# Kernel optimization log

Measured on AMD Instinct MI355X. Metric: run time of the kernel, lower is better.

## Reference

```python
import jax, jax.numpy as jnp
import numpy as np

N_NODES = 100000
N_EDGES = 1600000
D_IN, D_HID, D_OUT = 128, 128, 64


def spmm(row, col, val, h, n):
    # y[i] = sum_{e: row[e]==i} val[e] * h[col[e]]  (A_hat @ h with A in COO form)
    return jax.ops.segment_sum(val[:, None] * h[col], row, num_segments=n)


def setup_inputs() -> dict:
    key = jax.random.key(0)
    ks = jax.random.split(key, 7)
    x = jax.random.normal(ks[0], (1, N_NODES, D_IN), dtype=jnp.float32)
    edge_row = jax.random.randint(ks[1], (N_EDGES,), 0, N_NODES, dtype=jnp.int32)
    edge_col = jax.random.randint(ks[2], (N_EDGES,), 0, N_NODES, dtype=jnp.int32)
    edge_val = jax.random.uniform(ks[3], (N_EDGES,), dtype=jnp.float32)
    W0 = jax.random.normal(ks[4], (D_HID, D_IN), dtype=jnp.float32) * 0.05
    W1 = jax.random.normal(ks[5], (D_HID, D_HID), dtype=jnp.float32) * 0.05
    W2 = jax.random.normal(ks[6], (D_OUT, D_HID), dtype=jnp.float32) * 0.05
    return {"x": x, "edge_row": edge_row, "edge_col": edge_col,
            "edge_val": edge_val, "W0": W0, "W1": W1, "W2": W2}


def reference(x, edge_row, edge_col, edge_val, W0, W1, W2):
    B, N, D = x.shape
    n = B * N
    h = x.reshape(n, D)
    # input conv: Linear (no bias) -> SpMM -> ReLU
    h = jax.nn.relu(spmm(edge_row, edge_col, edge_val, h @ W0.T, n))
    # hidden conv with residual: ReLU(A (h W1^T)) + h
    h = jax.nn.relu(spmm(edge_row, edge_col, edge_val, h @ W1.T, n)) + h
    # dropout is identity in eval mode
    out = spmm(edge_row, edge_col, edge_val, h @ W2.T, n)
    return out
```

## Files before the change

### kernel.cpp

```cpp
#include <hip/hip_runtime.h>


typedef unsigned int u32;
typedef unsigned short u16;
typedef __attribute__((ext_vector_type(8))) short bf16x8;
typedef __attribute__((ext_vector_type(4))) float f32x4;

constexpr int NN = 100000;
constexpr int NE = 1600000;
constexpr int PAD = 100352;
constexpr int NBUCK = 392;
constexpr int BCAP = 4608;
constexpr int EPB = 4096;
constexpr int P1B = (NE + EPB - 1) / EPB;
constexpr int G0B = (NN + 63) / 64;
constexpr int NCB = 13;

__device__ __forceinline__ u16 f2bf(float f) {
    u32 x = __float_as_uint(f);
    x += 0x7fffu + ((x >> 16) & 1u);
    return (u16)(x >> 16);
}

__device__ __forceinline__ void wfrag_one(const float* __restrict__ W,
                                          u16* __restrict__ Wf, int total, int i)
{
    if (i < total) {
        const int j    = i & 7;
        const int lane = (i >> 3) & 63;
        const int kc   = (i >> 9) & 3;
        const int ct   = i >> 11;
        const int src  = (ct * 16 + (lane & 15)) * 128 + kc * 32 + (lane >> 4) * 8 + j;
        Wf[i] = f2bf(W[src]);
    }
}

__global__ __launch_bounds__(256)
void wcvt_kernel(const float* __restrict__ W0, const float* __restrict__ W1,
                 const float* __restrict__ W2, u16* __restrict__ wf0,
                 u16* __restrict__ wf1, u16* __restrict__ wf2)
{
    const int i = blockIdx.x * 256 + threadIdx.x;
    wfrag_one(W0, wf0, 128 * 128, i);
    wfrag_one(W1, wf1, 128 * 128, i);
    wfrag_one(W2, wf2, 64 * 128, i);
}

__global__ __launch_bounds__(256)
void part1_kernel(const int* __restrict__ erow, const int* __restrict__ ecol,
                  const float* __restrict__ eval,
                  int2* __restrict__ part, int* __restrict__ boffs)
{
    __shared__ int shist[512];
    __shared__ int sexcl[512];
    __shared__ int sdat[256];
    const int tid = threadIdx.x;
    const int blk = blockIdx.x;

    shist[tid] = 0; shist[tid + 256] = 0;
    __syncthreads();

    const int base = blk * EPB;
    int rr[EPB / 256];
    #pragma unroll
    for (int j = 0; j < EPB / 256; ++j) {
        const int e = base + j * 256 + tid;
        rr[j] = (e < NE) ? erow[e] : -1;
        if (rr[j] >= 0) atomicAdd(&shist[rr[j] >> 8], 1);
    }
    __syncthreads();

    const int c0 = shist[2 * tid];
    const int c1 = shist[2 * tid + 1];
    const int tsum = c0 + c1;
    sdat[tid] = tsum;
    __syncthreads();
    #pragma unroll
    for (int off = 1; off < 256; off <<= 1) {
        const int v = (tid >= off) ? sdat[tid - off] : 0;
        __syncthreads();
        sdat[tid] += v;
        __syncthreads();
    }
    const int excl = sdat[tid] - tsum;
    sexcl[2 * tid]     = excl;
    sexcl[2 * tid + 1] = excl + c0;
    __syncthreads();

    for (int b = tid; b < NBUCK; b += 256)
        boffs[(size_t)b * P1B + blk] = sexcl[b];
    if (tid == 0) boffs[(size_t)NBUCK * P1B + blk] = sdat[255];
    __syncthreads();

    #pragma unroll
    for (int j = 0; j < EPB / 256; ++j) {
        const int r = rr[j];
        if (r >= 0) {
            const int e = base + j * 256 + tid;
            const int pos = atomicAdd(&sexcl[r >> 8], 1);
            part[(size_t)blk * EPB + pos] =
                make_int2(((r & 255) << 17) | ecol[e], __float_as_int(eval[e]));
        }
    }
}

__global__ __launch_bounds__(256)
void gemm0_kernel(const float* __restrict__ x, const u16* __restrict__ Wf,
                  u16* __restrict__ Cb)
{
    constexpr int RS   = 136;
    constexpr int PADW = 136;
    __shared__ u16 smem[64 * 136];
    u16* sA = smem;
    u16* sC = smem;
    const int tid  = threadIdx.x;
    const int w    = tid >> 6;
    const int lane = tid & 63;
    const int m    = lane & 15;
    const int q    = lane >> 4;
    const int rowBase = (int)blockIdx.x * 64;

    #pragma unroll
    for (int i = 0; i < 8; ++i) {
        const int g = (i * 256 + tid) * 4;
        const int r = g >> 7, c = g & 127;
        float4 v = make_float4(0.f, 0.f, 0.f, 0.f);
        if (rowBase + r < NN) v = *(const float4*)(x + (size_t)(rowBase + r) * 128 + c);
        u16* d = &sA[r * RS + c];
        d[0] = f2bf(v.x); d[1] = f2bf(v.y); d[2] = f2bf(v.z); d[3] = f2bf(v.w);
    }
    __syncthreads();

    bf16x8 afrag[4];
    #pragma unroll
    for (int kc = 0; kc < 4; ++kc)
        afrag[kc] = *(const bf16x8*)&sA[(w * 16 + m) * RS + kc * 32 + q * 8];
    __syncthreads();

    #pragma unroll
    for (int ct = 0; ct < 8; ++ct) {
        f32x4 acc = {0.f, 0.f, 0.f, 0.f};
        #pragma unroll
        for (int kc = 0; kc < 4; ++kc) {
            const bf16x8 b = *(const bf16x8*)(Wf + (((ct * 4 + kc) * 64) + lane) * 8);
            acc = __builtin_amdgcn_mfma_f32_16x16x32_bf16(afrag[kc], b, acc, 0, 0, 0);
        }
        #pragma unroll
        for (int r = 0; r < 4; ++r)
            sC[(w * 16 + q * 4 + r) * PADW + ct * 16 + m] = f2bf(acc[r]);
    }
    __syncthreads();

    const int g    = lane >> 2;
    const int cb   = (lane & 3) * 32;
    const int grow = rowBase + w * 16 + g;
    if (grow < NN) {
        #pragma unroll
        for (int i = 0; i < 4; ++i) {
            const int4 v = *(const int4*)&sC[(w * 16 + g) * PADW + cb + i * 8];
            *(int4*)(Cb + (size_t)grow * 128 + cb + i * 8) = v;
        }
    }
}

__global__ __launch_bounds__(256)
void bsum_kernel(const int* __restrict__ boffs, int* __restrict__ bcur)
{
    __shared__ int sdata[256];
    const int b = blockIdx.x;
    const int tid = threadIdx.x;
    int s = 0;
    for (int k = tid; k < P1B; k += 256)
        s += boffs[(size_t)(b + 1) * P1B + k] - boffs[(size_t)b * P1B + k];
    sdata[tid] = s;
    __syncthreads();
    #pragma unroll
    for (int off = 128; off > 0; off >>= 1) {
        if (tid < off) sdata[tid] += sdata[tid + off];
        __syncthreads();
    }
    if (tid == 0) bcur[b] = sdata[0];
}

__global__ __launch_bounds__(256)
void part2_kernel(const int* __restrict__ bcur, const int* __restrict__ boffs,
                  const int2* __restrict__ part,
                  int* __restrict__ offs, int2* __restrict__ pce)
{
    __shared__ int2 sbuf[BCAP];
    __shared__ int scnt[256 * NCB];
    __shared__ int slo[512];
    __shared__ int sinc[512];
    __shared__ int sdata[256];
    const int b = blockIdx.x;
    const int tid = threadIdx.x;

    int partial = 0;
    for (int i = tid; i < b; i += 256) partial += bcur[i];
    sdata[tid] = partial;
    __syncthreads();
    #pragma unroll
    for (int off = 128; off > 0; off >>= 1) {
        if (tid < off) sdata[tid] += sdata[tid + off];
        __syncthreads();
    }
    const int gb = sdata[0];
    const int cnt = bcur[b];
    __syncthreads();

    {
        int k = tid;
        int l0 = 0, ln = 0;
        if (k < P1B) {
            l0 = boffs[(size_t)b * P1B + k];
            ln = boffs[(size_t)(b + 1) * P1B + k] - l0;
        }
        slo[k] = l0; sinc[k] = ln;
        k = tid + 256; l0 = 0; ln = 0;
        if (k < P1B) {
            l0 = boffs[(size_t)b * P1B + k];
            ln = boffs[(size_t)(b + 1) * P1B + k] - l0;
        }
        slo[k] = l0; sinc[k] = ln;
    }
    #pragma unroll
    for (int j = 0; j < NCB; ++j) scnt[j * 256 + tid] = 0;
    __syncthreads();

    for (int off = 1; off < 512; off <<= 1) {
        const int v0 = (tid >= off) ? sinc[tid - off] : 0;
        const int v1 = (tid + 256 >= off) ? sinc[tid + 256 - off] : 0;
        __syncthreads();
        sinc[tid]       += v0;
        sinc[tid + 256] += v1;
        __syncthreads();
    }

    for (int i = tid; i < cnt; i += 256) {
        int k = 0;
        #pragma unroll
        for (int step = 256; step > 0; step >>= 1) {
            const int nk = k + step;
            if (nk <= 511 && sinc[nk - 1] <= i) k = nk;
        }
        const int loc = i - (k ? sinc[k - 1] : 0);
        sbuf[i] = part[(size_t)k * EPB + slo[k] + loc];
    }
    __syncthreads();

    for (int i = tid; i < cnt; i += 256) {
        const int xk = sbuf[i].x;
        atomicAdd(&scnt[(((u32)xk) >> 17) * NCB + ((xk & 0x1FFFF) >> 13)], 1);
    }
    __syncthreads();

    int rsum = 0;
    #pragma unroll
    for (int j = 0; j < NCB; ++j) rsum += scnt[tid * NCB + j];
    sdata[tid] = rsum;
    __syncthreads();
    #pragma unroll
    for (int off = 1; off < 256; off <<= 1) {
        const int v = (tid >= off) ? sdata[tid - off] : 0;
        __syncthreads();
        sdata[tid] += v;
        __syncthreads();
    }
    const int excl = sdata[tid] - rsum;
    offs[b * 256 + tid] = gb + excl;

    int run = gb + excl;
    #pragma unroll
    for (int j = 0; j < NCB; ++j) {
        const int c = scnt[tid * NCB + j];
        scnt[tid * NCB + j] = run;
        run += c;
    }
    __syncthreads();

    for (int i = tid; i < cnt; i += 256) {
        const int2 ev = sbuf[i];
        const int pos = atomicAdd(
            &scnt[(((u32)ev.x) >> 17) * NCB + ((ev.x & 0x1FFFF) >> 13)], 1);
        pce[pos] = make_int2(ev.x & 0x1FFFF, ev.y);
    }
}

template<int LPC>
__device__ __forceinline__ void load_row(const u16* p, u32* u) {
    if constexpr (LPC == 8) {
        const uint4 t = *(const uint4*)p;
        u[0] = t.x; u[1] = t.y; u[2] = t.z; u[3] = t.w;
    } else {
        const uint2 t = *(const uint2*)p;
        u[0] = t.x; u[1] = t.y;
    }
}

template<int LPC>
__device__ __forceinline__ void fma_row(float v, const u32* u, float* a) {
    #pragma unroll
    for (int j = 0; j < LPC / 2; ++j) {
        a[2*j]   = fmaf(v, __uint_as_float(u[j] << 16),         a[2*j]);
        a[2*j+1] = fmaf(v, __uint_as_float(u[j] & 0xffff0000u), a[2*j+1]);
    }
}

template<int DO, int MODE>
__global__ __launch_bounds__(256)
void spmm_gemm(const int* __restrict__ offs, const int2* __restrict__ pce,
               const u16* __restrict__ Hb, const u16* __restrict__ Wf,
               const u16* __restrict__ Res, u16* __restrict__ Cb,
               u16* __restrict__ Hout)
{
    constexpr int RS   = 136;
    constexpr int PADW = DO + 8;
    __shared__ u16 smem[16 * 136];
    const int tid = threadIdx.x;
    const int ln  = tid & 15;
    const int rl  = tid >> 4;
    const int row = blockIdx.x * 16 + rl;

    const int s = offs[row];
    const int t = offs[row + 1];
    const u16* hbase = Hb + ln * 8;

    float a0[8], a1[8];
    #pragma unroll
    for (int j = 0; j < 8; ++j) { a0[j] = 0.f; a1[j] = 0.f; }

    for (int e = s; e < t; e += 16) {
        int2 my = make_int2(0, 0);
        if (e + ln < t) my = pce[e + ln];
        const int rem = t - e;
        #pragma unroll
        for (int qd = 0; qd < 4; ++qd) {
            if (qd * 4 < rem) {
                const int c0 = __shfl(my.x, qd * 4 + 0, 16);
                const int v0 = __shfl(my.y, qd * 4 + 0, 16);
                const int c1 = __shfl(my.x, qd * 4 + 1, 16);
                const int v1 = __shfl(my.y, qd * 4 + 1, 16);
                const int c2 = __shfl(my.x, qd * 4 + 2, 16);
                const int v2 = __shfl(my.y, qd * 4 + 2, 16);
                const int c3 = __shfl(my.x, qd * 4 + 3, 16);
                const int v3 = __shfl(my.y, qd * 4 + 3, 16);
                u32 u0[4], u1[4], u2[4], u3[4];
                load_row<8>(hbase + (size_t)c0 * 128, u0);
                load_row<8>(hbase + (size_t)c1 * 128, u1);
                load_row<8>(hbase + (size_t)c2 * 128, u2);
                load_row<8>(hbase + (size_t)c3 * 128, u3);
                fma_row<8>(__int_as_float(v0), u0, a0);
                fma_row<8>(__int_as_float(v1), u1, a1);
                fma_row<8>(__int_as_float(v2), u2, a0);
                fma_row<8>(__int_as_float(v3), u3, a1);
            }
        }
    }
    #pragma unroll
    for (int j = 0; j < 8; ++j) a0[j] = fmaxf(a0[j] + a1[j], 0.f);

    if constexpr (MODE == 2) {
        u32 r[4];
        load_row<8>(Res + (size_t)row * 128 + ln * 8, r);
        #pragma unroll
        for (int j = 0; j < 4; ++j) {
            a0[2*j]   += __uint_as_float(r[j] << 16);
            a0[2*j+1] += __uint_as_float(r[j] & 0xffff0000u);
        }
    }
    u32 o[4];
    #pragma unroll
    for (int j = 0; j < 4; ++j)
        o[j] = (u32)f2bf(a0[2*j]) | ((u32)f2bf(a0[2*j+1]) << 16);
    const uint4 packed = make_uint4(o[0], o[1], o[2], o[3]);
    *(uint4*)&smem[rl * RS + ln * 8] = packed;
    if constexpr (MODE == 1)
        *(uint4*)(Hout + (size_t)row * 128 + ln * 8) = packed;
    __syncthreads();

    constexpr int TPW = DO / 64;
    const int w    = tid >> 6;
    const int lane = tid & 63;
    const int m    = lane & 15;
    const int q    = lane >> 4;

    bf16x8 afrag[4];
    #pragma unroll
    for (int kc = 0; kc < 4; ++kc)
        afrag[kc] = *(const bf16x8*)&smem[m * RS + kc * 32 + q * 8];

    f32x4 acc[TPW];
    #pragma unroll
    for (int tw = 0; tw < TPW; ++tw) {
        const int ct = w * TPW + tw;
        acc[tw] = (f32x4){0.f, 0.f, 0.f, 0.f};
        #pragma unroll
        for (int kc = 0; kc < 4; ++kc) {
            const bf16x8 b = *(const bf16x8*)(Wf + (((ct * 4 + kc) * 64) + lane) * 8);
            acc[tw] = __builtin_amdgcn_mfma_f32_16x16x32_bf16(afrag[kc], b, acc[tw], 0, 0, 0);
        }
    }
    __syncthreads();

    #pragma unroll
    for (int tw = 0; tw < TPW; ++tw) {
        const int ct = w * TPW + tw;
        #pragma unroll
        for (int r = 0; r < 4; ++r)
            smem[(q * 4 + r) * PADW + ct * 16 + m] = f2bf(acc[tw][r]);
    }
    __syncthreads();

    if (DO == 128 || tid < 128) {
        const int g = tid * 8;
        const int r = g / DO;
        const int c = g % DO;
        const int4 v = *(const int4*)&smem[r * PADW + c];
        *(int4*)(Cb + ((size_t)blockIdx.x * 16 + r) * DO + c) = v;
    }
}

__global__ __launch_bounds__(256)
void spmm_out(const int* __restrict__ offs, const int2* __restrict__ pce,
              const u16* __restrict__ Hb, float* __restrict__ Y)
{
    const int ln  = threadIdx.x & 15;
    const int row = blockIdx.x * 16 + (threadIdx.x >> 4);
    if (row >= NN) return;
    const int s = offs[row];
    const int t = offs[row + 1];
    const u16* hbase = Hb + ln * 4;

    float a0[4], a1[4];
    #pragma unroll
    for (int j = 0; j < 4; ++j) { a0[j] = 0.f; a1[j] = 0.f; }

    for (int e = s; e < t; e += 16) {
        int2 my = make_int2(0, 0);
        if (e + ln < t) my = pce[e + ln];
        const int rem = t - e;
        #pragma unroll
        for (int qd = 0; qd < 4; ++qd) {
            if (qd * 4 < rem) {
                const int c0 = __shfl(my.x, qd * 4 + 0, 16);
                const int v0 = __shfl(my.y, qd * 4 + 0, 16);
                const int c1 = __shfl(my.x, qd * 4 + 1, 16);
                const int v1 = __shfl(my.y, qd * 4 + 1, 16);
                const int c2 = __shfl(my.x, qd * 4 + 2, 16);
                const int v2 = __shfl(my.y, qd * 4 + 2, 16);
                const int c3 = __shfl(my.x, qd * 4 + 3, 16);
                const int v3 = __shfl(my.y, qd * 4 + 3, 16);
                u32 u0[2], u1[2], u2[2], u3[2];
                load_row<4>(hbase + (size_t)c0 * 64, u0);
                load_row<4>(hbase + (size_t)c1 * 64, u1);
                load_row<4>(hbase + (size_t)c2 * 64, u2);
                load_row<4>(hbase + (size_t)c3 * 64, u3);
                fma_row<4>(__int_as_float(v0), u0, a0);
                fma_row<4>(__int_as_float(v1), u1, a1);
                fma_row<4>(__int_as_float(v2), u2, a0);
                fma_row<4>(__int_as_float(v3), u3, a1);
            }
        }
    }
    #pragma unroll
    for (int j = 0; j < 4; ++j) a0[j] += a1[j];
    *(float4*)(Y + (size_t)row * 64 + ln * 4) = make_float4(a0[0], a0[1], a0[2], a0[3]);
}

extern "C" void kernel_launch(void* const* d_in, const int* in_sizes, int n_in,
                              void* d_out, int out_size, void* d_ws, size_t ws_size,
                              hipStream_t stream) {
    const float* x    = (const float*)d_in[0];
    const int*   erow = (const int*)  d_in[1];
    const int*   ecol = (const int*)  d_in[2];
    const float* eval = (const float*)d_in[3];
    const float* W0   = (const float*)d_in[4];
    const float* W1   = (const float*)d_in[5];
    const float* W2   = (const float*)d_in[6];
    float* out = (float*)d_out;

    char* p = (char*)d_ws;
    const size_t BUFB = (size_t)NN * 128 * sizeof(u16);
    u16* t0b  = (u16*)p;  p += BUFB;
    u16* t1b  = (u16*)p;  p += BUFB;
    u16* h1b  = (u16*)p;  p += BUFB;
    u16* wf0  = (u16*)p;  p += 128 * 128 * 2;
    u16* wf1  = (u16*)p;  p += 128 * 128 * 2;
    u16* wf2  = (u16*)p;  p += 64 * 128 * 2;
    int* bcur   = (int*)p; p += 512 * 4;
    int* boffs  = (int*)p; p += (size_t)(NBUCK + 1) * P1B * 4;
    int* offs   = (int*)p; p += ((size_t)PAD + 256) * 4;
    int2* part  = (int2*)p; p += (size_t)P1B * EPB * 8;
    int2* pce   = (int2*)p;

    const dim3 blk(256);
    const int rowBlocks = NN / 16;

    wcvt_kernel <<<64, blk, 0, stream>>>(W0, W1, W2, wf0, wf1, wf2);
    part1_kernel<<<P1B, blk, 0, stream>>>(erow, ecol, eval, part, boffs);
    gemm0_kernel<<<G0B, blk, 0, stream>>>(x, wf0, t0b);
    bsum_kernel <<<NBUCK, blk, 0, stream>>>(boffs, bcur);
    part2_kernel<<<NBUCK, blk, 0, stream>>>(bcur, boffs, part, offs, pce);
    spmm_gemm<128, 1><<<rowBlocks, blk, 0, stream>>>(offs, pce, t0b, wf1, nullptr, t1b, h1b);
    spmm_gemm<64, 2><<<rowBlocks, blk, 0, stream>>>(offs, pce, t1b, wf2, h1b, t0b, nullptr);
    spmm_out<<<rowBlocks, blk, 0, stream>>>(offs, pce, t0b, out);
}
```

Baseline: 337.8 us.

## Fuse partition and gemm0 kernels, drop bsum, use 128-row buckets

Merges the edge partition pass and the first dense GEMM into one launch, with block-index ranges choosing the role. The separate bucket-sum kernel is removed and its work folded into part2, which now computes the bucket base and count directly from boffs. Buckets shrink from 256 to 128 rows, doubling the bucket count to 784 and cutting per-block shared memory in part2, which should give more parallelism and occupancy. In exchange part1 builds a larger histogram, boffs grows, and part2 blocks each run two extra reductions.

```diff
diff --git a/kernel.cpp b/kernel.cpp
--- a/kernel.cpp
+++ b/kernel.cpp
@@ -8,13 +8,15 @@
 
 constexpr int NN = 100000;
 constexpr int NE = 1600000;
+constexpr int RPB = 128;
+constexpr int NBUCK = 784;
 constexpr int PAD = 100352;
-constexpr int NBUCK = 392;
-constexpr int BCAP = 4608;
+constexpr int BCAP = 2432;
 constexpr int EPB = 4096;
 constexpr int P1B = (NE + EPB - 1) / EPB;
 constexpr int G0B = (NN + 63) / 64;
 constexpr int NCB = 13;
+constexpr int HB  = 1024;
 
 __device__ __forceinline__ u16 f2bf(float f) {
     u32 x = __float_as_uint(f);
@@ -47,78 +49,79 @@
 }
 
 __global__ __launch_bounds__(256)
-void part1_kernel(const int* __restrict__ erow, const int* __restrict__ ecol,
-                  const float* __restrict__ eval,
-                  int2* __restrict__ part, int* __restrict__ boffs)
+void k1_kernel(const float* __restrict__ x, const u16* __restrict__ Wf,
+               u16* __restrict__ Cb,
+               const int* __restrict__ erow, const int* __restrict__ ecol,
+               const float* __restrict__ eval,
+               int2* __restrict__ part, int* __restrict__ boffs)
 {
-    __shared__ int shist[512];
-    __shared__ int sexcl[512];
-    __shared__ int sdat[256];
+    __shared__ u16 smem[64 * 136];
     const int tid = threadIdx.x;
-    const int blk = blockIdx.x;
-
-    shist[tid] = 0; shist[tid + 256] = 0;
-    __syncthreads();
-
-    const int base = blk * EPB;
-    int rr[EPB / 256];
-    #pragma unroll
-    for (int j = 0; j < EPB / 256; ++j) {
-        const int e = base + j * 256 + tid;
-        rr[j] = (e < NE) ? erow[e] : -1;
-        if (rr[j] >= 0) atomicAdd(&shist[rr[j] >> 8], 1);
-    }
-    __syncthreads();
-
-    const int c0 = shist[2 * tid];
-    const int c1 = shist[2 * tid + 1];
-    const int tsum = c0 + c1;
-    sdat[tid] = tsum;
-    __syncthreads();
-    #pragma unroll
-    for (int off = 1; off < 256; off <<= 1) {
-        const int v = (tid >= off) ? sdat[tid - off] : 0;
-        __syncthreads();
-        sdat[tid] += v;
-        __syncthreads();
-    }
-    const int excl = sdat[tid] - tsum;
-    sexcl[2 * tid]     = excl;
-    sexcl[2 * tid + 1] = excl + c0;
-    __syncthreads();
-
-    for (int b = tid; b < NBUCK; b += 256)
-        boffs[(size_t)b * P1B + blk] = sexcl[b];
-    if (tid == 0) boffs[(size_t)NBUCK * P1B + blk] = sdat[255];
-    __syncthreads();
-
-    #pragma unroll
-    for (int j = 0; j < EPB / 256; ++j) {
-        const int r = rr[j];
-        if (r >= 0) {
+
+    if ((int)blockIdx.x < P1B) {
+        int* shist = (int*)smem;
+        int* sexcl = shist + HB;
+        int* sdat  = sexcl + HB;
+        const int blk = blockIdx.x;
+
+        #pragma unroll
+        for (int j = 0; j < HB / 256; ++j) shist[j * 256 + tid] = 0;
+        __syncthreads();
+
+        const int base = blk * EPB;
+        int rr[EPB / 256];
+        #pragma unroll
+        for (int j = 0; j < EPB / 256; ++j) {
             const int e = base + j * 256 + tid;
-            const int pos = atomicAdd(&sexcl[r >> 8], 1);
-            part[(size_t)blk * EPB + pos] =
-                make_int2(((r & 255) << 17) | ecol[e], __float_as_int(eval[e]));
-        }
-    }
-}
-
-__global__ __launch_bounds__(256)
-void gemm0_kernel(const float* __restrict__ x, const u16* __restrict__ Wf,
-                  u16* __restrict__ Cb)
-{
+            rr[j] = (e < NE) ? erow[e] : -1;
+            if (rr[j] >= 0) atomicAdd(&shist[rr[j] >> 7], 1);
+        }
+        __syncthreads();
+
+        int c[4]; int tsum = 0;
+        #pragma unroll
+        for (int i = 0; i < 4; ++i) { c[i] = shist[tid * 4 + i]; tsum += c[i]; }
+        sdat[tid] = tsum;
+        __syncthreads();
+        #pragma unroll
+        for (int off = 1; off < 256; off <<= 1) {
+            const int v = (tid >= off) ? sdat[tid - off] : 0;
+            __syncthreads();
+            sdat[tid] += v;
+            __syncthreads();
+        }
+        int run = sdat[tid] - tsum;
+        #pragma unroll
+        for (int i = 0; i < 4; ++i) { sexcl[tid * 4 + i] = run; run += c[i]; }
+        __syncthreads();
+
+        for (int b = tid; b < NBUCK; b += 256)
+            boffs[(size_t)b * P1B + blk] = sexcl[b];
+        if (tid == 0) boffs[(size_t)NBUCK * P1B + blk] = sdat[255];
+        __syncthreads();
+
+        #pragma unroll
+        for (int j = 0; j < EPB / 256; ++j) {
+            const int r = rr[j];
+            if (r >= 0) {
+                const int e = base + j * 256 + tid;
+                const int pos = atomicAdd(&sexcl[r >> 7], 1);
+                part[(size_t)blk * EPB + pos] =
+                    make_int2(((r & 127) << 17) | ecol[e], __float_as_int(eval[e]));
+            }
+        }
+        return;
+    }
+
     constexpr int RS   = 136;
     constexpr int PADW = 136;
-    __shared__ u16 smem[64 * 136];
     u16* sA = smem;
     u16* sC = smem;
-    const int tid  = threadIdx.x;
     const int w    = tid >> 6;
     const int lane = tid & 63;
     const int m    = lane & 15;
     const int q    = lane >> 4;
-    const int rowBase = (int)blockIdx.x * 64;
+    const int rowBase = ((int)blockIdx.x - P1B) * 64;
 
     #pragma unroll
     for (int i = 0; i < 8; ++i) {
@@ -164,50 +167,22 @@
 }
 
 __global__ __launch_bounds__(256)
-void bsum_kernel(const int* __restrict__ boffs, int* __restrict__ bcur)
-{
-    __shared__ int sdata[256];
-    const int b = blockIdx.x;
-    const int tid = threadIdx.x;
-    int s = 0;
-    for (int k = tid; k < P1B; k += 256)
-        s += boffs[(size_t)(b + 1) * P1B + k] - boffs[(size_t)b * P1B + k];
-    sdata[tid] = s;
-    __syncthreads();
-    #pragma unroll
-    for (int off = 128; off > 0; off >>= 1) {
-        if (tid < off) sdata[tid] += sdata[tid + off];
-        __syncthreads();
-    }
-    if (tid == 0) bcur[b] = sdata[0];
-}
-
-__global__ __launch_bounds__(256)
-void part2_kernel(const int* __restrict__ bcur, const int* __restrict__ boffs,
-                  const int2* __restrict__ part,
+void part2_kernel(const int* __restrict__ boffs, const int2* __restrict__ part,
                   int* __restrict__ offs, int2* __restrict__ pce)
 {
     __shared__ int2 sbuf[BCAP];
-    __shared__ int scnt[256 * NCB];
+    __shared__ int scnt[RPB * NCB];
     __shared__ int slo[512];
     __shared__ int sinc[512];
     __shared__ int sdata[256];
     const int b = blockIdx.x;
     const int tid = threadIdx.x;
 
-    int partial = 0;
-    for (int i = tid; i < b; i += 256) partial += bcur[i];
-    sdata[tid] = partial;
-    __syncthreads();
-    #pragma unroll
-    for (int off = 128; off > 0; off >>= 1) {
-        if (tid < off) sdata[tid] += sdata[tid + off];
-        __syncthreads();
-    }
-    const int gb = sdata[0];
-    const int cnt = bcur[b];
-    __syncthreads();
-
+    int s0 = 0, s1 = 0;
+    for (int k = tid; k < P1B; k += 256) {
+        s0 += boffs[(size_t)b * P1B + k];
+        s1 += boffs[(size_t)(b + 1) * P1B + k];
+    }
     {
         int k = tid;
         int l0 = 0, ln = 0;
@@ -223,8 +198,26 @@
         }
         slo[k] = l0; sinc[k] = ln;
     }
-    #pragma unroll
-    for (int j = 0; j < NCB; ++j) scnt[j * 256 + tid] = 0;
+    sdata[tid] = s0;
+    __syncthreads();
+    #pragma unroll
+    for (int off = 128; off > 0; off >>= 1) {
+        if (tid < off) sdata[tid] += sdata[tid + off];
+        __syncthreads();
+    }
+    const int gb = sdata[0];
+    __syncthreads();
+    sdata[tid] = s1;
+    __syncthreads();
+    #pragma unroll
+    for (int off = 128; off > 0; off >>= 1) {
+        if (tid < off) sdata[tid] += sdata[tid + off];
+        __syncthreads();
+    }
+    const int cnt = sdata[0] - gb;
+    __syncthreads();
+
+    for (int j = tid; j < RPB * NCB; j += 256) scnt[j] = 0;
     __syncthreads();
 
     for (int off = 1; off < 512; off <<= 1) {
@@ -255,8 +248,10 @@
     __syncthreads();
 
     int rsum = 0;
-    #pragma unroll
-    for (int j = 0; j < NCB; ++j) rsum += scnt[tid * NCB + j];
+    if (tid < RPB) {
+        #pragma unroll
+        for (int j = 0; j < NCB; ++j) rsum += scnt[tid * NCB + j];
+    }
     sdata[tid] = rsum;
     __syncthreads();
     #pragma unroll
@@ -267,14 +262,15 @@
         __syncthreads();
     }
     const int excl = sdata[tid] - rsum;
-    offs[b * 256 + tid] = gb + excl;
-
-    int run = gb + excl;
-    #pragma unroll
-    for (int j = 0; j < NCB; ++j) {
-        const int c = scnt[tid * NCB + j];
-        scnt[tid * NCB + j] = run;
-        run += c;
+    if (tid < RPB) {
+        offs[b * RPB + tid] = gb + excl;
+        int run = gb + excl;
+        #pragma unroll
+        for (int j = 0; j < NCB; ++j) {
+            const int c = scnt[tid * NCB + j];
+            scnt[tid * NCB + j] = run;
+            run += c;
+        }
     }
     __syncthreads();
 
@@ -487,7 +483,6 @@
     u16* wf0  = (u16*)p;  p += 128 * 128 * 2;
     u16* wf1  = (u16*)p;  p += 128 * 128 * 2;
     u16* wf2  = (u16*)p;  p += 64 * 128 * 2;
-    int* bcur   = (int*)p; p += 512 * 4;
     int* boffs  = (int*)p; p += (size_t)(NBUCK + 1) * P1B * 4;
     int* offs   = (int*)p; p += ((size_t)PAD + 256) * 4;
     int2* part  = (int2*)p; p += (size_t)P1B * EPB * 8;
@@ -496,11 +491,9 @@
     const dim3 blk(256);
     const int rowBlocks = NN / 16;
 
-    wcvt_kernel <<<64, blk, 0, stream>>>(W0, W1, W2, wf0, wf1, wf2);
-    part1_kernel<<<P1B, blk, 0, stream>>>(erow, ecol, eval, part, boffs);
-    gemm0_kernel<<<G0B, blk, 0, stream>>>(x, wf0, t0b);
-    bsum_kernel <<<NBUCK, blk, 0, stream>>>(boffs, bcur);
-    part2_kernel<<<NBUCK, blk, 0, stream>>>(bcur, boffs, part, offs, pce);
+    wcvt_kernel<<<64, blk, 0, stream>>>(W0, W1, W2, wf0, wf1, wf2);
+    k1_kernel  <<<P1B + G0B, blk, 0, stream>>>(x, wf0, t0b, erow, ecol, eval, part, boffs);
+    part2_kernel<<<NBUCK, blk, 0, stream>>>(boffs, part, offs, pce);
     spmm_gemm<128, 1><<<rowBlocks, blk, 0, stream>>>(offs, pce, t0b, wf1, nullptr, t1b, h1b);
     spmm_gemm<64, 2><<<rowBlocks, blk, 0, stream>>>(offs, pce, t1b, wf2, h1b, t0b, nullptr);
     spmm_out<<<rowBlocks, blk, 0, stream>>>(offs, pce, t0b, out);
```

Measured after the change: 319.1 us. -5.5%, faster.
